# Performance work log

Hardware: AMD Instinct MI355X
Metric: run time of the kernel (lower is better)

## Reference

```python
import jax, jax.numpy as jnp
import numpy as np

NBITS = 16  # posit word size passed to posit_forward
ES = 1      # posit exponent-field size (standard posit16 uses es=1)


def posit_quant(x, nbits=NBITS, es=ES):
    """Round-trip float -> posit(nbits, es) -> float, vectorized.

    Emulates posit quantization: regime length determines how many fraction
    bits remain, mantissa is rounded to that precision, magnitude clamped to
    [minpos, maxpos]. Straight-through estimator keeps gradients useful.
    """
    absx = jnp.abs(x)
    sign = jnp.sign(x)
    safe = jnp.maximum(absx, 1e-30)
    scale = jnp.floor(jnp.log2(safe))                 # binary exponent
    useed_log2 = float(2 ** es)
    regime = jnp.floor(scale / useed_log2)
    rlen = jnp.where(regime >= 0, regime + 2.0, 1.0 - regime)  # regime bits
    fbits = jnp.clip(nbits - 1 - es - rlen, 0.0, 28.0)          # fraction bits left
    pw = jnp.exp2(fbits)
    m = safe * jnp.exp2(-scale)                       # mantissa in [1, 2)
    mq = 1.0 + jnp.round((m - 1.0) * pw) / pw
    maxscale = float((nbits - 2) * (2 ** es))         # maxpos = 2^((n-2)*2^es)
    mag = jnp.clip(mq * jnp.exp2(scale), jnp.exp2(-maxscale), jnp.exp2(maxscale))
    q = jnp.where(absx == 0.0, 0.0, sign * mag)
    return x + jax.lax.stop_gradient(q - x)           # straight-through


def posit_linear(x, W, b):
    # posit_forward: quantize operands, GEMM, quantize the accumulated output
    xq = posit_quant(x)
    Wq = posit_quant(W)
    bq = posit_quant(b)
    return posit_quant(xq @ Wq.T + bq)


def setup_inputs() -> dict:
    key = jax.random.key(0)
    ks = jax.random.split(key, 7)

    def w(k, o, i):
        return jax.random.normal(k, (o, i), jnp.float32) * (1.0 / np.sqrt(i))

    return {
        "x": jax.random.normal(ks[0], (4096, 2048), jnp.float32),
        "W0": w(ks[1], 8192, 2048),
        "b0": jax.random.normal(ks[2], (8192,), jnp.float32) * 0.01,
        "W1": w(ks[3], 8192, 8192),
        "b1": jax.random.normal(ks[4], (8192,), jnp.float32) * 0.01,
        "W2": w(ks[5], 2048, 8192),
        "b2": jax.random.normal(ks[6], (2048,), jnp.float32) * 0.01,
    }


def reference(x, W0, b0, W1, b1, W2, b2):
    # layer 0: posit linear + relu (clamp(min=0))
    h = jax.nn.relu(posit_linear(x, W0, b0))
    # layer 1: posit linear + relu
    h = jax.nn.relu(posit_linear(h, W1, b1))
    # layer 2: posit linear, identity activation
    return posit_linear(h, W2, b2)
```

## Files before the change

### kernel.cpp

```cpp
#include <hip/hip_runtime.h>
#include <hip/hip_bf16.h>
#include <cstdint>
#include <cstddef>

using bf16 = __hip_bfloat16;
typedef __attribute__((ext_vector_type(8))) short short8;
typedef __attribute__((ext_vector_type(4))) float f32x4;

__device__ __forceinline__ float posit_quant_f32(float x) {
  float absx = fabsf(x);
  float safe = fmaxf(absx, 1e-30f);
  uint32_t bits = __float_as_uint(safe);
  int scale = (int)((bits >> 23) & 0xFFu) - 127;
  int regime = scale >> 1;
  int rlen = (regime >= 0) ? (regime + 2) : (1 - regime);
  int fbits = 14 - rlen;
  fbits = fbits < 0 ? 0 : fbits;
  float pw = (float)(1 << fbits);
  float m = __uint_as_float((bits & 0x007FFFFFu) | 0x3F800000u);
  float mq = rintf((m - 1.0f) * pw) * (1.0f / pw) + 1.0f;
  float mag = mq * __uint_as_float((uint32_t)(scale + 127) << 23);
  mag = fminf(fmaxf(mag, 0x1p-28f), 0x1p28f);
  return (absx == 0.0f) ? 0.0f : copysignf(mag, x);
}

__global__ void kquant_bf16(const float* __restrict__ in, bf16* __restrict__ out, long n4) {
  long i = (long)blockIdx.x * blockDim.x + threadIdx.x;
  long stride = (long)gridDim.x * blockDim.x;
  for (; i < n4; i += stride) {
    float4 v = ((const float4*)in)[i];
    ushort4 o;
    o.x = __builtin_bit_cast(unsigned short, __float2bfloat16(posit_quant_f32(v.x)));
    o.y = __builtin_bit_cast(unsigned short, __float2bfloat16(posit_quant_f32(v.y)));
    o.z = __builtin_bit_cast(unsigned short, __float2bfloat16(posit_quant_f32(v.z)));
    o.w = __builtin_bit_cast(unsigned short, __float2bfloat16(posit_quant_f32(v.w)));
    ((ushort4*)out)[i] = o;
  }
}

__global__ void kcombine(const float* __restrict__ p, const float* __restrict__ bias,
                         float* __restrict__ out, long n4, long halfn, int cmask) {
  long i = (long)blockIdx.x * blockDim.x + threadIdx.x;
  long stride = (long)gridDim.x * blockDim.x;
  for (; i < n4; i += stride) {
    float4 a = ((const float4*)p)[i];
    float4 b = ((const float4*)(p + halfn))[i];
    int c0 = (int)(i & cmask) * 4;
    float4 o;
    o.x = posit_quant_f32(a.x + b.x + posit_quant_f32(bias[c0 + 0]));
    o.y = posit_quant_f32(a.y + b.y + posit_quant_f32(bias[c0 + 1]));
    o.z = posit_quant_f32(a.z + b.z + posit_quant_f32(bias[c0 + 2]));
    o.w = posit_quant_f32(a.w + b.w + posit_quant_f32(bias[c0 + 3]));
    ((float4*)out)[i] = o;
  }
}

typedef __attribute__((address_space(1))) uint32_t gu32;
typedef __attribute__((address_space(3))) uint32_t lu32;

#define SBAR()  do { __builtin_amdgcn_sched_barrier(0); __builtin_amdgcn_s_barrier(); \
                     __builtin_amdgcn_sched_barrier(0); } while (0)
#define LGKM0() do { asm volatile("s_waitcnt lgkmcnt(0)" ::: "memory"); \
                     __builtin_amdgcn_sched_barrier(0); } while (0)
#define VMCNT(N) asm volatile("s_waitcnt vmcnt(" #N ")" ::: "memory")

#define STG(SRC, KT, H, DST) do { \
    const char* _s = (SRC) + (long)((H) * 128) * Kb + (long)(KT) * 128; \
    char* _d = smem + (DST) + (H) * 16384 + wave * 1024; \
    __builtin_amdgcn_global_load_lds((const gu32*)_s, (lu32*)_d, 16, 0, 0); \
    __builtin_amdgcn_global_load_lds((const gu32*)(_s + 64 * Kb), (lu32*)(_d + 8192), 16, 0, 0); \
  } while (0)

#define LDA8(AOFF, FI, CK) (*(const short8*)(smem + (AOFF) + aRel + (FI) * 2048 + (CK)))
#define LDB8(BOFF, FJ, CK) (*(const short8*)(smem + (BOFF) + bRel + (FJ) * 2048 + (CK)))

#define BB0 98304
#define BB1 131072

#define MQ(FI0, FJ0) do { \
    _Pragma("unroll") \
    for (int fi = 0; fi < 4; ++fi) { \
      _Pragma("unroll") \
      for (int fj = 0; fj < 2; ++fj) { \
        acc[(FI0) + fi][(FJ0) + fj] = __builtin_amdgcn_mfma_f32_16x16x32_bf16( \
            afr[fi][0], bfr[(FJ0) + fj][0], acc[(FI0) + fi][(FJ0) + fj], 0, 0, 0); \
        acc[(FI0) + fi][(FJ0) + fj] = __builtin_amdgcn_mfma_f32_16x16x32_bf16( \
            afr[fi][1], bfr[(FJ0) + fj][1], acc[(FI0) + fi][(FJ0) + fj], 0, 0, 0); \
      } \
    } \
  } while (0)

template <int MODE>
__global__ __launch_bounds__(512, 2) void gemm256_posit(
    const bf16* __restrict__ A, const bf16* __restrict__ B,
    const float* __restrict__ bias, void* __restrict__ out,
    int M, int N, int Kfull, int Kloop, int nbt, int cpx) {
  __shared__ __align__(1024) char smem[163840];

  const int tid  = threadIdx.x;
  const int lane = tid & 63;
  const int wave = tid >> 6;
  const int wr = wave >> 2;
  const int wc = wave & 3;

  const int flat = blockIdx.x;
  const int wgid = (flat & 7) * cpx + (flat >> 3);
  const int split = wgid / nbt;
  const int t = wgid - split * nbt;
  const int nbx = N >> 8;
  const long brow0 = (long)(t / nbx) * 256;
  const long bcol0 = (long)(t % nbx) * 256;

  const long Kb = (long)Kfull * 2;
  const long splitoff = (long)split * Kloop * 2;

  const int srow = tid >> 3;
  const int scb  = ((tid & 7) * 16) ^ (((tid >> 3) & 7) << 4);
  const char* srcA = (const char*)A + (brow0 + srow) * Kb + scb + splitoff;
  const char* srcB = (const char*)B + (bcol0 + srow) * Kb + scb + splitoff;

  const int fr  = lane & 15;
  const int swz = (lane & 7) << 4;
  const int ck0 = (((lane >> 4) << 4)) ^ swz;
  const int ck1 = (64 + ((lane >> 4) << 4)) ^ swz;
  const int aRel = wr * 16384 + fr * 128;
  const int bRel = wc * 8192 + fr * 128;

  f32x4 acc[8][4] = {};
  short8 afr[4][2], bfr[4][2];

  const int nkt = Kloop >> 6;
  const int np  = nkt >> 1;

  int a0 = 0, a1 = 32768, a2 = 65536;

  STG(srcA, 0, 0, 0);     STG(srcA, 0, 1, 0);
  STG(srcB, 0, 0, BB0);   STG(srcB, 0, 1, BB0);
  STG(srcA, 1, 0, 32768); STG(srcA, 1, 1, 32768);
  STG(srcB, 1, 0, BB1);   STG(srcB, 1, 1, BB1);
  VMCNT(8);
  SBAR();

#pragma unroll 1
  for (int i = 0; i < np; ++i) {
    const int kS2 = (2 * i + 2) & (nkt - 1);
    const int kS3 = (2 * i + 3) & (nkt - 1);

#pragma unroll
    for (int f = 0; f < 4; ++f) { afr[f][0] = LDA8(a0, f, ck0); afr[f][1] = LDA8(a0, f, ck1); }
#pragma unroll
    for (int f = 0; f < 2; ++f) { bfr[f][0] = LDB8(BB0, f, ck0); bfr[f][1] = LDB8(BB0, f, ck1); }
    STG(srcA, kS2, 0, a2);
    SBAR(); LGKM0();
    __builtin_amdgcn_s_setprio(1); MQ(0, 0); __builtin_amdgcn_s_setprio(0);
    SBAR();

#pragma unroll
    for (int f = 2; f < 4; ++f) { bfr[f][0] = LDB8(BB0, f, ck0); bfr[f][1] = LDB8(BB0, f, ck1); }
    STG(srcA, kS2, 1, a2);
    SBAR(); LGKM0();
    __builtin_amdgcn_s_setprio(1); MQ(0, 2); __builtin_amdgcn_s_setprio(0);
    SBAR();

#pragma unroll
    for (int f = 0; f < 4; ++f) { afr[f][0] = LDA8(a0, f + 4, ck0); afr[f][1] = LDA8(a0, f + 4, ck1); }
    STG(srcB, kS2, 0, BB0);
    SBAR(); LGKM0();
    __builtin_amdgcn_s_setprio(1); MQ(4, 0); __builtin_amdgcn_s_setprio(0);
    SBAR();

    STG(srcB, kS2, 1, BB0);
    VMCNT(8);
    SBAR();
    __builtin_amdgcn_s_setprio(1); MQ(4, 2); __builtin_amdgcn_s_setprio(0);
    SBAR();

#pragma unroll
    for (int f = 0; f < 4; ++f) { afr[f][0] = LDA8(a1, f, ck0); afr[f][1] = LDA8(a1, f, ck1); }
#pragma unroll
    for (int f = 0; f < 2; ++f) { bfr[f][0] = LDB8(BB1, f, ck0); bfr[f][1] = LDB8(BB1, f, ck1); }
    STG(srcA, kS3, 0, a0);
    SBAR(); LGKM0();
    __builtin_amdgcn_s_setprio(1); MQ(0, 0); __builtin_amdgcn_s_setprio(0);
    SBAR();

#pragma unroll
    for (int f = 2; f < 4; ++f) { bfr[f][0] = LDB8(BB1, f, ck0); bfr[f][1] = LDB8(BB1, f, ck1); }
    STG(srcA, kS3, 1, a0);
    SBAR(); LGKM0();
    __builtin_amdgcn_s_setprio(1); MQ(0, 2); __builtin_amdgcn_s_setprio(0);
    SBAR();

#pragma unroll
    for (int f = 0; f < 4; ++f) { afr[f][0] = LDA8(a1, f + 4, ck0); afr[f][1] = LDA8(a1, f + 4, ck1); }
    STG(srcB, kS3, 0, BB1);
    SBAR(); LGKM0();
    __builtin_amdgcn_s_setprio(1); MQ(4, 0); __builtin_amdgcn_s_setprio(0);
    SBAR();

    STG(srcB, kS3, 1, BB1);
    VMCNT(8);
    SBAR();
    __builtin_amdgcn_s_setprio(1); MQ(4, 2); __builtin_amdgcn_s_setprio(0);
    SBAR();

    int tmp = a2; a2 = a1; a1 = a0; a0 = tmp;
  }
  asm volatile("s_waitcnt vmcnt(0)" ::: "memory");

  const int orow = (lane >> 4) * 4;
  const long row0 = brow0 + wr * 128;
  const long col0 = bcol0 + wc * 64;
  const long obase = (MODE == 2) ? (long)split * M * N : 0;
#pragma unroll
  for (int fj = 0; fj < 4; ++fj) {
    const long col = col0 + fj * 16 + fr;
    const float bv = (MODE == 2) ? 0.0f : posit_quant_f32(bias[col]);
#pragma unroll
    for (int fi = 0; fi < 8; ++fi) {
#pragma unroll
      for (int q = 0; q < 4; ++q) {
        float v = acc[fi][fj][q];
        if (MODE != 2) {
          v = posit_quant_f32(v + bv);
          if (MODE == 0) v = fmaxf(v, 0.0f);
        }
        const long idx = obase + (row0 + fi * 16 + orow + q) * (long)N + col;
        if (MODE == 0) ((bf16*)out)[idx] = __float2bfloat16(v);
        else           ((float*)out)[idx] = v;
      }
    }
  }
}

#define GBM 128
#define GBN 128
#define GBK 32

__device__ __forceinline__ void gload_lds16(const void* g, void* l) {
  __builtin_amdgcn_global_load_lds((const gu32*)g, (lu32*)l, 16, 0, 0);
}

template <bool RELU, bool OUTBF16>
__global__ __launch_bounds__(256, 2) void gemm_bt_posit(
    const bf16* __restrict__ A, const bf16* __restrict__ B,
    const float* __restrict__ bias, void* __restrict__ out,
    int M, int N, int K) {
  __shared__ __align__(1024) bf16 sA[GBM][GBK];
  __shared__ __align__(1024) bf16 sB[GBN][GBK];

  const int tid = threadIdx.x;
  const int lane = tid & 63;
  const int wave = tid >> 6;
  const int wr = wave >> 1;
  const int wc = wave & 1;
  const long brow0 = (long)blockIdx.y * GBM;
  const long bcol0 = (long)blockIdx.x * GBN;

  const int srow = lane >> 2;
  const int scol = (lane & 3) * 8;
  const int seg0 = wave * 2;

  const bf16* gA0 = A + (brow0 + seg0 * 16 + srow) * (long)K + scol;
  const bf16* gA1 = A + (brow0 + seg0 * 16 + 16 + srow) * (long)K + scol;
  const bf16* gB0 = B + (bcol0 + seg0 * 16 + srow) * (long)K + scol;
  const bf16* gB1 = B + (bcol0 + seg0 * 16 + 16 + srow) * (long)K + scol;
  bf16* lA0 = (bf16*)sA + seg0 * 512;
  bf16* lA1 = lA0 + 512;
  bf16* lB0 = (bf16*)sB + seg0 * 512;
  bf16* lB1 = lB0 + 512;

  f32x4 acc[4][4] = {};
  const int fr = lane & 15;
  const int fk = (lane >> 4) * 8;

  for (int kt = 0; kt < K; kt += GBK) {
    __syncthreads();
    gload_lds16(gA0 + kt, lA0);
    gload_lds16(gA1 + kt, lA1);
    gload_lds16(gB0 + kt, lB0);
    gload_lds16(gB1 + kt, lB1);
    __syncthreads();

    short8 af[4], bfv[4];
#pragma unroll
    for (int i = 0; i < 4; ++i) af[i] = *(const short8*)&sA[wr * 64 + i * 16 + fr][fk];
#pragma unroll
    for (int j = 0; j < 4; ++j) bfv[j] = *(const short8*)&sB[wc * 64 + j * 16 + fr][fk];
#pragma unroll
    for (int i = 0; i < 4; ++i)
#pragma unroll
      for (int j = 0; j < 4; ++j)
        acc[i][j] = __builtin_amdgcn_mfma_f32_16x16x32_bf16(af[i], bfv[j], acc[i][j], 0, 0, 0);
  }

  const int orow = (lane >> 4) * 4;
  const long row0 = brow0 + wr * 64;
  const long col0 = bcol0 + wc * 64;
#pragma unroll
  for (int j = 0; j < 4; ++j) {
    const long col = col0 + j * 16 + fr;
    const float bv = posit_quant_f32(bias[col]);
#pragma unroll
    for (int i = 0; i < 4; ++i) {
#pragma unroll
      for (int q = 0; q < 4; ++q) {
        float v = posit_quant_f32(acc[i][j][q] + bv);
        if (RELU) v = fmaxf(v, 0.0f);
        const long idx = (row0 + i * 16 + orow + q) * (long)N + col;
        if (OUTBF16) ((bf16*)out)[idx] = __float2bfloat16(v);
        else         ((float*)out)[idx] = v;
      }
    }
  }
}

extern "C" void kernel_launch(void* const* d_in, const int* in_sizes, int n_in,
                              void* d_out, int out_size, void* d_ws, size_t ws_size,
                              hipStream_t stream) {
  const float* x  = (const float*)d_in[0];
  const float* W0 = (const float*)d_in[1];
  const float* b0 = (const float*)d_in[2];
  const float* W1 = (const float*)d_in[3];
  const float* b1 = (const float*)d_in[4];
  const float* W2 = (const float*)d_in[5];
  const float* b2 = (const float*)d_in[6];

  const int M = 4096, D0 = 2048, D1 = 8192, D2 = 8192, DO = 2048;

  char* ws = (char*)d_ws;
  size_t off = 0;
  auto alloc = [&](size_t bytes) {
    char* p = ws + off;
    off += (bytes + 255) & ~(size_t)255;
    return p;
  };
  bf16* xq  = (bf16*)alloc((size_t)M * D0 * 2);
  bf16* W0q = (bf16*)alloc((size_t)D1 * D0 * 2);
  bf16* W1q = (bf16*)alloc((size_t)D2 * D1 * 2);
  bf16* W2q = (bf16*)alloc((size_t)DO * D2 * 2);
  bf16* h0  = (bf16*)alloc((size_t)M * D1 * 2);
  bf16* h1  = (bf16*)alloc((size_t)M * D2 * 2);
  float* part = (float*)alloc((size_t)2 * M * DO * 4);
  const bool splitk = (off <= ws_size);
  (void)in_sizes; (void)n_in; (void)out_size;

  auto quant = [&](const float* in, bf16* outp, long n) {
    long n4 = n / 4;
    long want = (n4 + 255) / 256;
    int blocks = (int)(want < 2048 ? want : 2048);
    kquant_bf16<<<blocks, 256, 0, stream>>>(in, outp, n4);
  };
  quant(x,  xq,  (long)M * D0);
  quant(W0, W0q, (long)D1 * D0);
  quant(W1, W1q, (long)D2 * D1);
  quant(W2, W2q, (long)DO * D2);

  {
    int nbt = (D1 / 256) * (M / 256), nwg = nbt;
    gemm256_posit<0><<<dim3(nwg), dim3(512), 0, stream>>>(
        xq, W0q, b0, h0, M, D1, D0, D0, nbt, nwg / 8);
  }
  {
    int nbt = (D2 / 256) * (M / 256), nwg = nbt;
    gemm256_posit<0><<<dim3(nwg), dim3(512), 0, stream>>>(
        h0, W1q, b1, h1, M, D2, D1, D1, nbt, nwg / 8);
  }
  if (splitk) {
    int nbt = (DO / 256) * (M / 256);
    int nwg = nbt * 2;
    gemm256_posit<2><<<dim3(nwg), dim3(512), 0, stream>>>(
        h1, W2q, nullptr, part, M, DO, D2, D2 / 2, nbt, nwg / 8);
    long n4 = (long)M * DO / 4;
    kcombine<<<2048, 256, 0, stream>>>(part, b2, (float*)d_out, n4,
                                       (long)M * DO, DO / 4 - 1);
  } else {
    gemm_bt_posit<false, false><<<dim3(DO / GBN, M / GBM), dim3(256), 0, stream>>>(
        h1, W2q, b2, (float*)d_out, M, DO, D2);
  }
}
```

Measured before the change: 894.6 us.

## Switch 256x256 GEMM to 32x32x16 MFMA with double-buffered LDS

Replaces the 16x16x32 bf16 MFMA tiling with 32x32x16 MFMA, so each wave computes 4x2 blocks of 32x32 output using 16-float accumulators. The fragment-load swizzle and the epilogue row mapping are rewritten to match the new layout. The A operand moves from a triple buffer to a double buffer, shrinking LDS from 160KB to 128KB, and the prefetch order and vmcnt waits change accordingly. The goal is fewer MFMA issues and fewer LDS reads per FLOP. The risks are a shorter prefetch distance for A and extra register copies through the accp staging array.

```diff
diff --git a/kernel.cpp b/kernel.cpp
--- a/kernel.cpp
+++ b/kernel.cpp
@@ -6,6 +6,7 @@
 using bf16 = __hip_bfloat16;
 typedef __attribute__((ext_vector_type(8))) short short8;
 typedef __attribute__((ext_vector_type(4))) float f32x4;
+typedef __attribute__((ext_vector_type(16))) float f32x16;
 
 __device__ __forceinline__ float posit_quant_f32(float x) {
   float absx = fabsf(x);
@@ -64,6 +65,11 @@
                      __builtin_amdgcn_sched_barrier(0); } while (0)
 #define VMCNT(N) asm volatile("s_waitcnt vmcnt(" #N ")" ::: "memory")
 
+#define AB0 0
+#define AB1 32768
+#define BB0 65536
+#define BB1 98304
+
 #define STG(SRC, KT, H, DST) do { \
     const char* _s = (SRC) + (long)((H) * 128) * Kb + (long)(KT) * 128; \
     char* _d = smem + (DST) + (H) * 16384 + wave * 1024; \
@@ -71,21 +77,16 @@
     __builtin_amdgcn_global_load_lds((const gu32*)(_s + 64 * Kb), (lu32*)(_d + 8192), 16, 0, 0); \
   } while (0)
 
-#define LDA8(AOFF, FI, CK) (*(const short8*)(smem + (AOFF) + aRel + (FI) * 2048 + (CK)))
-#define LDB8(BOFF, FJ, CK) (*(const short8*)(smem + (BOFF) + bRel + (FJ) * 2048 + (CK)))
-
-#define BB0 98304
-#define BB1 131072
-
-#define MQ(FI0, FJ0) do { \
+#define LDA8(BUF, MB, KS) (*(const short8*)(smem + (BUF) + aRel + (MB) * 4096 + ck[KS]))
+#define LDB8(BUF, NB, KS) (*(const short8*)(smem + (BUF) + bRel + (NB) * 4096 + ck[KS]))
+
+#define MQ32(NB) do { \
     _Pragma("unroll") \
-    for (int fi = 0; fi < 4; ++fi) { \
+    for (int ks = 0; ks < 4; ++ks) { \
       _Pragma("unroll") \
-      for (int fj = 0; fj < 2; ++fj) { \
-        acc[(FI0) + fi][(FJ0) + fj] = __builtin_amdgcn_mfma_f32_16x16x32_bf16( \
-            afr[fi][0], bfr[(FJ0) + fj][0], acc[(FI0) + fi][(FJ0) + fj], 0, 0, 0); \
-        acc[(FI0) + fi][(FJ0) + fj] = __builtin_amdgcn_mfma_f32_16x16x32_bf16( \
-            afr[fi][1], bfr[(FJ0) + fj][1], acc[(FI0) + fi][(FJ0) + fj], 0, 0, 0); \
+      for (int mi = 0; mi < 2; ++mi) { \
+        accp[mi][NB] = __builtin_amdgcn_mfma_f32_32x32x16_bf16( \
+            afr[mi][ks], bfr[NB][ks], accp[mi][NB], 0, 0, 0); \
       } \
     } \
   } while (0)
@@ -95,7 +96,7 @@
     const bf16* __restrict__ A, const bf16* __restrict__ B,
     const float* __restrict__ bias, void* __restrict__ out,
     int M, int N, int Kfull, int Kloop, int nbt, int cpx) {
-  __shared__ __align__(1024) char smem[163840];
+  __shared__ __align__(1024) char smem[131072];
 
   const int tid  = threadIdx.x;
   const int lane = tid & 63;
@@ -119,113 +120,134 @@
   const char* srcA = (const char*)A + (brow0 + srow) * Kb + scb + splitoff;
   const char* srcB = (const char*)B + (bcol0 + srow) * Kb + scb + splitoff;
 
-  const int fr  = lane & 15;
-  const int swz = (lane & 7) << 4;
-  const int ck0 = (((lane >> 4) << 4)) ^ swz;
-  const int ck1 = (64 + ((lane >> 4) << 4)) ^ swz;
-  const int aRel = wr * 16384 + fr * 128;
-  const int bRel = wc * 8192 + fr * 128;
-
-  f32x4 acc[8][4] = {};
-  short8 afr[4][2], bfr[4][2];
+  const int r31 = lane & 31;
+  const int aRel = wr * 16384 + r31 * 128;
+  const int bRel = wc * 8192 + r31 * 128;
+  int ck[4];
+#pragma unroll
+  for (int ks = 0; ks < 4; ++ks)
+    ck[ks] = (ks << 5) ^ ((((lane >> 5) ^ (lane & 7)) << 4));
+
+  f32x16 accp[2][2] = {};
+  f32x16 acc[4][2] = {};
+  short8 afr[2][4], bfr[2][4];
 
   const int nkt = Kloop >> 6;
   const int np  = nkt >> 1;
 
-  int a0 = 0, a1 = 32768, a2 = 65536;
-
-  STG(srcA, 0, 0, 0);     STG(srcA, 0, 1, 0);
-  STG(srcB, 0, 0, BB0);   STG(srcB, 0, 1, BB0);
-  STG(srcA, 1, 0, 32768); STG(srcA, 1, 1, 32768);
-  STG(srcB, 1, 0, BB1);   STG(srcB, 1, 1, BB1);
-  VMCNT(8);
+  STG(srcB, 0, 0, BB0); STG(srcB, 0, 1, BB0);
+  STG(srcA, 0, 0, AB0); STG(srcA, 0, 1, AB0);
+  STG(srcB, 1, 0, BB1); STG(srcB, 1, 1, BB1);
+  VMCNT(4);
   SBAR();
 
 #pragma unroll 1
   for (int i = 0; i < np; ++i) {
+    const int kA1 = 2 * i + 1;
     const int kS2 = (2 * i + 2) & (nkt - 1);
     const int kS3 = (2 * i + 3) & (nkt - 1);
 
 #pragma unroll
-    for (int f = 0; f < 4; ++f) { afr[f][0] = LDA8(a0, f, ck0); afr[f][1] = LDA8(a0, f, ck1); }
-#pragma unroll
-    for (int f = 0; f < 2; ++f) { bfr[f][0] = LDB8(BB0, f, ck0); bfr[f][1] = LDB8(BB0, f, ck1); }
-    STG(srcA, kS2, 0, a2);
-    SBAR(); LGKM0();
-    __builtin_amdgcn_s_setprio(1); MQ(0, 0); __builtin_amdgcn_s_setprio(0);
-    SBAR();
-
-#pragma unroll
-    for (int f = 2; f < 4; ++f) { bfr[f][0] = LDB8(BB0, f, ck0); bfr[f][1] = LDB8(BB0, f, ck1); }
-    STG(srcA, kS2, 1, a2);
-    SBAR(); LGKM0();
-    __builtin_amdgcn_s_setprio(1); MQ(0, 2); __builtin_amdgcn_s_setprio(0);
-    SBAR();
-
-#pragma unroll
-    for (int f = 0; f < 4; ++f) { afr[f][0] = LDA8(a0, f + 4, ck0); afr[f][1] = LDA8(a0, f + 4, ck1); }
+    for (int ks = 0; ks < 4; ++ks) {
+      afr[0][ks] = LDA8(AB0, 0, ks); afr[1][ks] = LDA8(AB0, 1, ks);
+      bfr[0][ks] = LDB8(BB0, 0, ks);
+    }
+    STG(srcA, kA1, 0, AB1);
+    SBAR(); LGKM0();
+    accp[0][0] = acc[0][0]; accp[1][0] = acc[1][0];
+    __builtin_amdgcn_s_setprio(1); MQ32(0); __builtin_amdgcn_s_setprio(0);
+    acc[0][0] = accp[0][0]; acc[1][0] = accp[1][0];
+    SBAR();
+
+#pragma unroll
+    for (int ks = 0; ks < 4; ++ks) bfr[1][ks] = LDB8(BB0, 1, ks);
+    STG(srcA, kA1, 1, AB1);
+    SBAR(); LGKM0();
+    accp[0][1] = acc[0][1]; accp[1][1] = acc[1][1];
+    __builtin_amdgcn_s_setprio(1); MQ32(1); __builtin_amdgcn_s_setprio(0);
+    acc[0][1] = accp[0][1]; acc[1][1] = accp[1][1];
+    SBAR();
+
+#pragma unroll
+    for (int ks = 0; ks < 4; ++ks) {
+      afr[0][ks] = LDA8(AB0, 2, ks); afr[1][ks] = LDA8(AB0, 3, ks);
+    }
     STG(srcB, kS2, 0, BB0);
     SBAR(); LGKM0();
-    __builtin_amdgcn_s_setprio(1); MQ(4, 0); __builtin_amdgcn_s_setprio(0);
+    accp[0][0] = acc[2][0]; accp[1][0] = acc[3][0];
+    __builtin_amdgcn_s_setprio(1); MQ32(0); __builtin_amdgcn_s_setprio(0);
+    acc[2][0] = accp[0][0]; acc[3][0] = accp[1][0];
     SBAR();
 
     STG(srcB, kS2, 1, BB0);
-    VMCNT(8);
-    SBAR();
-    __builtin_amdgcn_s_setprio(1); MQ(4, 2); __builtin_amdgcn_s_setprio(0);
-    SBAR();
-
-#pragma unroll
-    for (int f = 0; f < 4; ++f) { afr[f][0] = LDA8(a1, f, ck0); afr[f][1] = LDA8(a1, f, ck1); }
-#pragma unroll
-    for (int f = 0; f < 2; ++f) { bfr[f][0] = LDB8(BB1, f, ck0); bfr[f][1] = LDB8(BB1, f, ck1); }
-    STG(srcA, kS3, 0, a0);
-    SBAR(); LGKM0();
-    __builtin_amdgcn_s_setprio(1); MQ(0, 0); __builtin_amdgcn_s_setprio(0);
-    SBAR();
-
-#pragma unroll
-    for (int f = 2; f < 4; ++f) { bfr[f][0] = LDB8(BB1, f, ck0); bfr[f][1] = LDB8(BB1, f, ck1); }
-    STG(srcA, kS3, 1, a0);
-    SBAR(); LGKM0();
-    __builtin_amdgcn_s_setprio(1); MQ(0, 2); __builtin_amdgcn_s_setprio(0);
-    SBAR();
-
-#pragma unroll
-    for (int f = 0; f < 4; ++f) { afr[f][0] = LDA8(a1, f + 4, ck0); afr[f][1] = LDA8(a1, f + 4, ck1); }
+    VMCNT(4);
+    SBAR();
+    accp[0][1] = acc[2][1]; accp[1][1] = acc[3][1];
+    __builtin_amdgcn_s_setprio(1); MQ32(1); __builtin_amdgcn_s_setprio(0);
+    acc[2][1] = accp[0][1]; acc[3][1] = accp[1][1];
+    SBAR();
+
+#pragma unroll
+    for (int ks = 0; ks < 4; ++ks) {
+      afr[0][ks] = LDA8(AB1, 0, ks); afr[1][ks] = LDA8(AB1, 1, ks);
+      bfr[0][ks] = LDB8(BB1, 0, ks);
+    }
+    STG(srcA, kS2, 0, AB0);
+    SBAR(); LGKM0();
+    accp[0][0] = acc[0][0]; accp[1][0] = acc[1][0];
+    __builtin_amdgcn_s_setprio(1); MQ32(0); __builtin_amdgcn_s_setprio(0);
+    acc[0][0] = accp[0][0]; acc[1][0] = accp[1][0];
+    SBAR();
+
+#pragma unroll
+    for (int ks = 0; ks < 4; ++ks) bfr[1][ks] = LDB8(BB1, 1, ks);
+    STG(srcA, kS2, 1, AB0);
+    SBAR(); LGKM0();
+    accp[0][1] = acc[0][1]; accp[1][1] = acc[1][1];
+    __builtin_amdgcn_s_setprio(1); MQ32(1); __builtin_amdgcn_s_setprio(0);
+    acc[0][1] = accp[0][1]; acc[1][1] = accp[1][1];
+    SBAR();
+
+#pragma unroll
+    for (int ks = 0; ks < 4; ++ks) {
+      afr[0][ks] = LDA8(AB1, 2, ks); afr[1][ks] = LDA8(AB1, 3, ks);
+    }
     STG(srcB, kS3, 0, BB1);
     SBAR(); LGKM0();
-    __builtin_amdgcn_s_setprio(1); MQ(4, 0); __builtin_amdgcn_s_setprio(0);
+    accp[0][0] = acc[2][0]; accp[1][0] = acc[3][0];
+    __builtin_amdgcn_s_setprio(1); MQ32(0); __builtin_amdgcn_s_setprio(0);
+    acc[2][0] = accp[0][0]; acc[3][0] = accp[1][0];
     SBAR();
 
     STG(srcB, kS3, 1, BB1);
-    VMCNT(8);
-    SBAR();
-    __builtin_amdgcn_s_setprio(1); MQ(4, 2); __builtin_amdgcn_s_setprio(0);
-    SBAR();
-
-    int tmp = a2; a2 = a1; a1 = a0; a0 = tmp;
+    VMCNT(4);
+    SBAR();
+    accp[0][1] = acc[2][1]; accp[1][1] = acc[3][1];
+    __builtin_amdgcn_s_setprio(1); MQ32(1); __builtin_amdgcn_s_setprio(0);
+    acc[2][1] = accp[0][1]; acc[3][1] = accp[1][1];
+    SBAR();
   }
   asm volatile("s_waitcnt vmcnt(0)" ::: "memory");
 
-  const int orow = (lane >> 4) * 4;
+  const int ohi = (lane >> 5) * 4;
   const long row0 = brow0 + wr * 128;
   const long col0 = bcol0 + wc * 64;
   const long obase = (MODE == 2) ? (long)split * M * N : 0;
 #pragma unroll
-  for (int fj = 0; fj < 4; ++fj) {
-    const long col = col0 + fj * 16 + fr;
+  for (int nb = 0; nb < 2; ++nb) {
+    const long col = col0 + nb * 32 + r31;
     const float bv = (MODE == 2) ? 0.0f : posit_quant_f32(bias[col]);
 #pragma unroll
-    for (int fi = 0; fi < 8; ++fi) {
-#pragma unroll
-      for (int q = 0; q < 4; ++q) {
-        float v = acc[fi][fj][q];
+    for (int mb = 0; mb < 4; ++mb) {
+#pragma unroll
+      for (int q = 0; q < 16; ++q) {
+        const int r = (q & 3) + 8 * (q >> 2) + ohi;
+        float v = acc[mb][nb][q];
         if (MODE != 2) {
           v = posit_quant_f32(v + bv);
           if (MODE == 0) v = fmaxf(v, 0.0f);
         }
-        const long idx = obase + (row0 + fi * 16 + orow + q) * (long)N + col;
+        const long idx = obase + (row0 + mb * 32 + r) * (long)N + col;
         if (MODE == 0) ((bf16*)out)[idx] = __float2bfloat16(v);
         else           ((float*)out)[idx] = v;
       }
```

Result: slower. 972.2 us (+8.7%).

## Shrink GEMM LDS ring to two stages and merge quant kernels into one

Applied to the files above, without the earlier changes.

The GEMM moves from a three-slot rotating A buffer (160 KB LDS) to fixed double buffers for A and B (128 KB), and changes the prefetch schedule so A runs one k-tile ahead instead of two, with tighter vmcnt waits. This cuts LDS use, which may allow more occupancy or fewer bank constraints, at the cost of less prefetch depth and more exposed load latency. Separately, the four quantization launches are fused into one grid-stride kernel that picks its source by index range, removing launch overhead and tail effects.

```diff
diff --git a/kernel.cpp b/kernel.cpp
--- a/kernel.cpp
+++ b/kernel.cpp
@@ -24,17 +24,30 @@
   return (absx == 0.0f) ? 0.0f : copysignf(mag, x);
 }
 
-__global__ void kquant_bf16(const float* __restrict__ in, bf16* __restrict__ out, long n4) {
+__device__ __forceinline__ ushort4 pq_bf16x4(float4 v) {
+  ushort4 o;
+  o.x = __builtin_bit_cast(unsigned short, __float2bfloat16(posit_quant_f32(v.x)));
+  o.y = __builtin_bit_cast(unsigned short, __float2bfloat16(posit_quant_f32(v.y)));
+  o.z = __builtin_bit_cast(unsigned short, __float2bfloat16(posit_quant_f32(v.z)));
+  o.w = __builtin_bit_cast(unsigned short, __float2bfloat16(posit_quant_f32(v.w)));
+  return o;
+}
+
+__global__ void kquant_all(const float* __restrict__ s0, bf16* __restrict__ d0,
+                           const float* __restrict__ s1, bf16* __restrict__ d1,
+                           const float* __restrict__ s2, bf16* __restrict__ d2,
+                           const float* __restrict__ s3, bf16* __restrict__ d3,
+                           long c0, long c1, long c2, long c3) {
   long i = (long)blockIdx.x * blockDim.x + threadIdx.x;
   long stride = (long)gridDim.x * blockDim.x;
-  for (; i < n4; i += stride) {
-    float4 v = ((const float4*)in)[i];
-    ushort4 o;
-    o.x = __builtin_bit_cast(unsigned short, __float2bfloat16(posit_quant_f32(v.x)));
-    o.y = __builtin_bit_cast(unsigned short, __float2bfloat16(posit_quant_f32(v.y)));
-    o.z = __builtin_bit_cast(unsigned short, __float2bfloat16(posit_quant_f32(v.z)));
-    o.w = __builtin_bit_cast(unsigned short, __float2bfloat16(posit_quant_f32(v.w)));
-    ((ushort4*)out)[i] = o;
+  for (; i < c3; i += stride) {
+    const float* s; bf16* d; long j;
+    if (i < c0)      { s = s0; d = d0; j = i; }
+    else if (i < c1) { s = s1; d = d1; j = i - c0; }
+    else if (i < c2) { s = s2; d = d2; j = i - c1; }
+    else             { s = s3; d = d3; j = i - c2; }
+    float4 v = ((const float4*)s)[j];
+    ((ushort4*)d)[j] = pq_bf16x4(v);
   }
 }
 
@@ -64,6 +77,11 @@
                      __builtin_amdgcn_sched_barrier(0); } while (0)
 #define VMCNT(N) asm volatile("s_waitcnt vmcnt(" #N ")" ::: "memory")
 
+#define AB0 0
+#define AB1 32768
+#define BB0 65536
+#define BB1 98304
+
 #define STG(SRC, KT, H, DST) do { \
     const char* _s = (SRC) + (long)((H) * 128) * Kb + (long)(KT) * 128; \
     char* _d = smem + (DST) + (H) * 16384 + wave * 1024; \
@@ -73,9 +91,6 @@
 
 #define LDA8(AOFF, FI, CK) (*(const short8*)(smem + (AOFF) + aRel + (FI) * 2048 + (CK)))
 #define LDB8(BOFF, FJ, CK) (*(const short8*)(smem + (BOFF) + bRel + (FJ) * 2048 + (CK)))
-
-#define BB0 98304
-#define BB1 131072
 
 #define MQ(FI0, FJ0) do { \
     _Pragma("unroll") \
@@ -95,7 +110,7 @@
     const bf16* __restrict__ A, const bf16* __restrict__ B,
     const float* __restrict__ bias, void* __restrict__ out,
     int M, int N, int Kfull, int Kloop, int nbt, int cpx) {
-  __shared__ __align__(1024) char smem[163840];
+  __shared__ __align__(1024) char smem[131072];
 
   const int tid  = threadIdx.x;
   const int lane = tid & 63;
@@ -132,79 +147,75 @@
   const int nkt = Kloop >> 6;
   const int np  = nkt >> 1;
 
-  int a0 = 0, a1 = 32768, a2 = 65536;
-
-  STG(srcA, 0, 0, 0);     STG(srcA, 0, 1, 0);
-  STG(srcB, 0, 0, BB0);   STG(srcB, 0, 1, BB0);
-  STG(srcA, 1, 0, 32768); STG(srcA, 1, 1, 32768);
-  STG(srcB, 1, 0, BB1);   STG(srcB, 1, 1, BB1);
-  VMCNT(8);
+  STG(srcB, 0, 0, BB0); STG(srcB, 0, 1, BB0);
+  STG(srcA, 0, 0, AB0); STG(srcA, 0, 1, AB0);
+  STG(srcB, 1, 0, BB1); STG(srcB, 1, 1, BB1);
+  VMCNT(4);
   SBAR();
 
 #pragma unroll 1
   for (int i = 0; i < np; ++i) {
+    const int kA1 = 2 * i + 1;
     const int kS2 = (2 * i + 2) & (nkt - 1);
     const int kS3 = (2 * i + 3) & (nkt - 1);
 
 #pragma unroll
-    for (int f = 0; f < 4; ++f) { afr[f][0] = LDA8(a0, f, ck0); afr[f][1] = LDA8(a0, f, ck1); }
+    for (int f = 0; f < 4; ++f) { afr[f][0] = LDA8(AB0, f, ck0); afr[f][1] = LDA8(AB0, f, ck1); }
 #pragma unroll
     for (int f = 0; f < 2; ++f) { bfr[f][0] = LDB8(BB0, f, ck0); bfr[f][1] = LDB8(BB0, f, ck1); }
-    STG(srcA, kS2, 0, a2);
+    STG(srcA, kA1, 0, AB1);
     SBAR(); LGKM0();
     __builtin_amdgcn_s_setprio(1); MQ(0, 0); __builtin_amdgcn_s_setprio(0);
     SBAR();
 
 #pragma unroll
     for (int f = 2; f < 4; ++f) { bfr[f][0] = LDB8(BB0, f, ck0); bfr[f][1] = LDB8(BB0, f, ck1); }
-    STG(srcA, kS2, 1, a2);
+    STG(srcA, kA1, 1, AB1);
     SBAR(); LGKM0();
     __builtin_amdgcn_s_setprio(1); MQ(0, 2); __builtin_amdgcn_s_setprio(0);
     SBAR();
 
 #pragma unroll
-    for (int f = 0; f < 4; ++f) { afr[f][0] = LDA8(a0, f + 4, ck0); afr[f][1] = LDA8(a0, f + 4, ck1); }
+    for (int f = 0; f < 4; ++f) { afr[f][0] = LDA8(AB0, f + 4, ck0); afr[f][1] = LDA8(AB0, f + 4, ck1); }
     STG(srcB, kS2, 0, BB0);
     SBAR(); LGKM0();
     __builtin_amdgcn_s_setprio(1); MQ(4, 0); __builtin_amdgcn_s_setprio(0);
     SBAR();
 
     STG(srcB, kS2, 1, BB0);
-    VMCNT(8);
+    VMCNT(4);
     SBAR();
     __builtin_amdgcn_s_setprio(1); MQ(4, 2); __builtin_amdgcn_s_setprio(0);
     SBAR();
 
 #pragma unroll
-    for (int f = 0; f < 4; ++f) { afr[f][0] = LDA8(a1, f, ck0); afr[f][1] = LDA8(a1, f, ck1); }
+    for (int f = 0; f < 4; ++f) { afr[f][0] = LDA8(AB1, f, ck0); afr[f][1] = LDA8(AB1, f, ck1); }
 #pragma unroll
     for (int f = 0; f < 2; ++f) { bfr[f][0] = LDB8(BB1, f, ck0); bfr[f][1] = LDB8(BB1, f, ck1); }
-    STG(srcA, kS3, 0, a0);
+    STG(srcA, kS2, 0, AB0);
     SBAR(); LGKM0();
     __builtin_amdgcn_s_setprio(1); MQ(0, 0); __builtin_amdgcn_s_setprio(0);
     SBAR();
 
 #pragma unroll
     for (int f = 2; f < 4; ++f) { bfr[f][0] = LDB8(BB1, f, ck0); bfr[f][1] = LDB8(BB1, f, ck1); }
-    STG(srcA, kS3, 1, a0);
+    STG(srcA, kS2, 1, AB0);
     SBAR(); LGKM0();
     __builtin_amdgcn_s_setprio(1); MQ(0, 2); __builtin_amdgcn_s_setprio(0);
     SBAR();
 
 #pragma unroll
-    for (int f = 0; f < 4; ++f) { afr[f][0] = LDA8(a1, f + 4, ck0); afr[f][1] = LDA8(a1, f + 4, ck1); }
+    for (int f = 0; f < 4; ++f) { afr[f][0] = LDA8(AB1, f + 4, ck0); afr[f][1] = LDA8(AB1, f + 4, ck1); }
     STG(srcB, kS3, 0, BB1);
     SBAR(); LGKM0();
     __builtin_amdgcn_s_setprio(1); MQ(4, 0); __builtin_amdgcn_s_setprio(0);
     SBAR();
 
     STG(srcB, kS3, 1, BB1);
-    VMCNT(8);
+    VMCNT(4);
     SBAR();
     __builtin_amdgcn_s_setprio(1); MQ(4, 2); __builtin_amdgcn_s_setprio(0);
     SBAR();
-
-    int tmp = a2; a2 = a1; a1 = a0; a0 = tmp;
   }
   asm volatile("s_waitcnt vmcnt(0)" ::: "memory");
 
@@ -345,16 +356,14 @@
   const bool splitk = (off <= ws_size);
   (void)in_sizes; (void)n_in; (void)out_size;
 
-  auto quant = [&](const float* in, bf16* outp, long n) {
-    long n4 = n / 4;
-    long want = (n4 + 255) / 256;
-    int blocks = (int)(want < 2048 ? want : 2048);
-    kquant_bf16<<<blocks, 256, 0, stream>>>(in, outp, n4);
-  };
-  quant(x,  xq,  (long)M * D0);
-  quant(W0, W0q, (long)D1 * D0);
-  quant(W1, W1q, (long)D2 * D1);
-  quant(W2, W2q, (long)DO * D2);
+  {
+    long q0 = (long)M * D0 / 4;
+    long q1 = q0 + (long)D1 * D0 / 4;
+    long q2 = q1 + (long)D2 * D1 / 4;
+    long q3 = q2 + (long)DO * D2 / 4;
+    kquant_all<<<2048, 256, 0, stream>>>(x, xq, W0, W0q, W1, W1q, W2, W2q,
+                                         q0, q1, q2, q3);
+  }
 
   {
     int nbt = (D1 / 256) * (M / 256), nwg = nbt;
```

New measurement: 888.5 us. About the same (-0.7%).
